# Kernel optimization log

Hardware: AMD Instinct MI355X
Metric: run time of the kernel (lower is better)

## Reference

```python
import jax, jax.numpy as jnp
import numpy as np

N = 33554432  # 2**25 activations, 128 MB fp32
K = 1024      # winners kept


def setup_inputs() -> dict:
    key = jax.random.key(0)
    inputs = jax.random.normal(key, (N,), dtype=jnp.float32)
    return {"inputs": inputs, "k": K}


def reference(inputs, k):
    # k-th largest value = threshold (original: tf.sort desc, take element k-1)
    topk_vals, _ = jax.lax.top_k(inputs, k)
    threshold = topk_vals[k - 1]
    # zero out everything strictly below the threshold
    return jnp.where(inputs < threshold, jnp.zeros_like(inputs), inputs)
```

## Files before the change

kernel.cpp:

```cpp
#include <hip/hip_runtime.h>
#include <stdint.h>


#define HIST_BINS 4096
#define CTRL_OFF  HIST_BINS
#define CAND_OFF  (HIST_BINS + 16)

typedef float f32x4 __attribute__((ext_vector_type(4)));

__device__ __forceinline__ uint32_t f2key(float x) {
  uint32_t u = __float_as_uint(x);
  return (u & 0x80000000u) ? ~u : (u | 0x80000000u);
}
__device__ __forceinline__ float key2f(uint32_t k) {
  uint32_t u = (k & 0x80000000u) ? (k & 0x7fffffffu) : ~k;
  return __uint_as_float(u);
}

__global__ void k_hist(const float4* __restrict__ in, int n4, int ntail,
                       const float* __restrict__ in_s,
                       uint32_t* __restrict__ ghist) {
  __shared__ uint32_t lh[HIST_BINS];
  for (int i = threadIdx.x; i < HIST_BINS; i += blockDim.x) lh[i] = 0;
  __syncthreads();
  int stride = gridDim.x * blockDim.x;
  for (int i = blockIdx.x * blockDim.x + threadIdx.x; i < n4; i += stride) {
    float4 v = in[i];
    atomicAdd(&lh[f2key(v.x) >> 20], 1u);
    atomicAdd(&lh[f2key(v.y) >> 20], 1u);
    atomicAdd(&lh[f2key(v.z) >> 20], 1u);
    atomicAdd(&lh[f2key(v.w) >> 20], 1u);
  }
  if (blockIdx.x == 0 && (int)threadIdx.x < ntail)
    atomicAdd(&lh[f2key(in_s[n4 * 4 + threadIdx.x]) >> 20], 1u);
  __syncthreads();
  for (int i = threadIdx.x; i < HIST_BINS; i += blockDim.x) {
    uint32_t c = lh[i];
    if (c) atomicAdd(&ghist[i], c);
  }
}

__global__ void k_select_bucket(const uint32_t* __restrict__ gh,
                                const int* __restrict__ kptr,
                                uint32_t* __restrict__ ctrl) {
  __shared__ uint32_t chunk[256];
  const int CPT = HIST_BINS / 256;
  int t = threadIdx.x;
  uint32_t s = 0;
  for (int i = 0; i < CPT; i++) s += gh[t * CPT + i];
  chunk[t] = s;
  __syncthreads();
  if (t == 0) {
    uint32_t K = (uint32_t)kptr[0];
    uint32_t above = 0;
    int sel = 0;
    for (int c = 255; c >= 0; c--) {
      if (above + chunk[c] >= K) { sel = c; break; }
      above += chunk[c];
    }
    int bsel = sel * CPT;
    for (int b = sel * CPT + CPT - 1; b >= sel * CPT; b--) {
      uint32_t c = gh[b];
      if (above + c >= K) { bsel = b; break; }
      above += c;
    }
    ctrl[1] = (uint32_t)bsel;
    ctrl[2] = K - above;
  }
}

__global__ void k_apply_gather(const float4* __restrict__ in,
                               float4* __restrict__ out, int n4, int ntail,
                               const float* __restrict__ in_s,
                               float* __restrict__ out_s,
                               uint32_t* __restrict__ ctrl,
                               uint32_t* __restrict__ keys,
                               uint32_t* __restrict__ idxs, uint32_t cap) {
  uint32_t sel = ctrl[1];
  int stride = gridDim.x * blockDim.x;
  for (int i = blockIdx.x * blockDim.x + threadIdx.x; i < n4; i += stride) {
    f32x4 vv = __builtin_nontemporal_load((const f32x4*)&in[i]);
    uint32_t k0 = f2key(vv.x), k1 = f2key(vv.y), k2 = f2key(vv.z), k3 = f2key(vv.w);
    uint32_t b0 = k0 >> 20, b1 = k1 >> 20, b2 = k2 >> 20, b3 = k3 >> 20;
    f32x4 r;
    r.x = (b0 > sel) ? vv.x : 0.0f;
    r.y = (b1 > sel) ? vv.y : 0.0f;
    r.z = (b2 > sel) ? vv.z : 0.0f;
    r.w = (b3 > sel) ? vv.w : 0.0f;
    if (b0 == sel) { uint32_t p = atomicAdd(&ctrl[0], 1u); if (p < cap) { keys[p] = k0; idxs[p] = 4u * i + 0u; } }
    if (b1 == sel) { uint32_t p = atomicAdd(&ctrl[0], 1u); if (p < cap) { keys[p] = k1; idxs[p] = 4u * i + 1u; } }
    if (b2 == sel) { uint32_t p = atomicAdd(&ctrl[0], 1u); if (p < cap) { keys[p] = k2; idxs[p] = 4u * i + 2u; } }
    if (b3 == sel) { uint32_t p = atomicAdd(&ctrl[0], 1u); if (p < cap) { keys[p] = k3; idxs[p] = 4u * i + 3u; } }
    __builtin_nontemporal_store(r, (f32x4*)&out[i]);
  }
  if (blockIdx.x == 0 && (int)threadIdx.x < ntail) {
    int j = n4 * 4 + threadIdx.x;
    float x = in_s[j];
    uint32_t kk = f2key(x);
    uint32_t bb = kk >> 20;
    out_s[j] = (bb > sel) ? x : 0.0f;
    if (bb == sel) { uint32_t p = atomicAdd(&ctrl[0], 1u); if (p < cap) { keys[p] = kk; idxs[p] = (uint32_t)j; } }
  }
}

__global__ void __launch_bounds__(1024) k_final(uint32_t* __restrict__ ctrl,
                                                const uint32_t* __restrict__ keys,
                                                const uint32_t* __restrict__ idxs,
                                                uint32_t cap,
                                                float* __restrict__ out_s) {
  __shared__ uint32_t sh[8192];
  __shared__ uint32_t cnt[16];
  __shared__ uint32_t s_p, s_want;
  int t = threadIdx.x;
  uint32_t n = ctrl[0]; if (n > cap) n = cap;
  bool useLds = (n <= 8192);
  if (useLds) for (uint32_t i = t; i < n; i += blockDim.x) sh[i] = keys[i];
  if (t == 0) { s_p = ctrl[1] << 20; s_want = ctrl[2]; }
  __syncthreads();
  uint32_t p = s_p;
  for (int d = 4; d >= 0; d--) {
    if (t < 16) cnt[t] = 0;
    __syncthreads();
    int sh_hi = 4 * d + 4;
    uint32_t pref = p >> sh_hi;
    for (uint32_t i = t; i < n; i += blockDim.x) {
      uint32_t kk = useLds ? sh[i] : keys[i];
      if ((kk >> sh_hi) == pref) atomicAdd(&cnt[(kk >> (4 * d)) & 15u], 1u);
    }
    __syncthreads();
    if (t == 0) {
      uint32_t want = s_want, acc = 0;
      uint32_t v = 0;
      for (int x = 15; x >= 0; x--) {
        if (acc + cnt[x] >= want) { v = (uint32_t)x; break; }
        acc += cnt[x];
      }
      s_p = p | (v << (4 * d));
      s_want = want - acc;
    }
    __syncthreads();
    p = s_p;
  }
  if (t == 0) ctrl[3] = __float_as_uint(key2f(p));
  for (uint32_t i = t; i < n; i += blockDim.x) {
    uint32_t kk = useLds ? sh[i] : keys[i];
    if (kk >= p) out_s[idxs[i]] = key2f(kk);
  }
}

extern "C" void kernel_launch(void* const* d_in, const int* in_sizes, int n_in,
                              void* d_out, int out_size, void* d_ws, size_t ws_size,
                              hipStream_t stream) {
  const float* in = (const float*)d_in[0];
  const int* kptr = (const int*)d_in[1];
  float* out = (float*)d_out;
  int n = in_sizes[0];
  int n4 = n >> 2;
  int ntail = n & 3;

  uint32_t* ws = (uint32_t*)d_ws;
  uint32_t* ghist = ws;
  uint32_t* ctrl = ws + CTRL_OFF;
  size_t ws_words = ws_size / 4;
  uint32_t cap = 0;
  if (ws_words > CAND_OFF + 2) cap = (uint32_t)((ws_words - CAND_OFF) / 2);
  uint32_t* keys = ws + CAND_OFF;
  uint32_t* idxs = keys + cap;

  hipMemsetAsync(d_ws, 0, CAND_OFF * sizeof(uint32_t), stream);

  k_hist<<<1024, 256, 0, stream>>>((const float4*)in, n4, ntail, in, ghist);
  k_select_bucket<<<1, 256, 0, stream>>>(ghist, kptr, ctrl);
  k_apply_gather<<<4096, 256, 0, stream>>>((const float4*)in, (float4*)out,
                                           n4, ntail, in, out, ctrl, keys, idxs, cap);
  k_final<<<1, 1024, 0, stream>>>(ctrl, keys, idxs, cap, out);
}
```

Before: 264.9 us.

## Fuse select and final kernels into preceding passes via last-block-done pattern

Merges the single-block bucket-select kernel into the histogram kernel and the single-block final refine kernel into the apply/gather kernel, using an atomic completion counter so the last finishing block does the serial work. It also rotates the global histogram flush order per block to spread atomic contention, changes the histogram launch to 512x512, and switches the apply pass input from a nontemporal load to a normal load. This removes two kernel launches and their gaps. In exchange, the final refinement now runs with 256 threads reading candidates from global memory instead of 1024 threads working from LDS.

```diff
diff --git a/kernel.cpp b/kernel.cpp
--- a/kernel.cpp
+++ b/kernel.cpp
@@ -17,10 +17,16 @@
   return __uint_as_float(u);
 }
 
-__global__ void k_hist(const float4* __restrict__ in, int n4, int ntail,
-                       const float* __restrict__ in_s,
-                       uint32_t* __restrict__ ghist) {
+__device__ __forceinline__ uint32_t agent_load(const uint32_t* p) {
+  return __hip_atomic_load(p, __ATOMIC_RELAXED, __HIP_MEMORY_SCOPE_AGENT);
+}
+
+__global__ void __launch_bounds__(512) k_hist_select(
+    const float4* __restrict__ in, int n4, int ntail,
+    const float* __restrict__ in_s, const int* __restrict__ kptr,
+    uint32_t* __restrict__ ghist, uint32_t* __restrict__ ctrl) {
   __shared__ uint32_t lh[HIST_BINS];
+  __shared__ uint32_t s_done;
   for (int i = threadIdx.x; i < HIST_BINS; i += blockDim.x) lh[i] = 0;
   __syncthreads();
   int stride = gridDim.x * blockDim.x;
@@ -35,32 +41,37 @@
     atomicAdd(&lh[f2key(in_s[n4 * 4 + threadIdx.x]) >> 20], 1u);
   __syncthreads();
   for (int i = threadIdx.x; i < HIST_BINS; i += blockDim.x) {
-    uint32_t c = lh[i];
-    if (c) atomicAdd(&ghist[i], c);
+    int j = (i + (blockIdx.x << 6)) & (HIST_BINS - 1);
+    uint32_t c = lh[j];
+    if (c) atomicAdd(&ghist[j], c);
   }
-}
+  __threadfence();
+  if (threadIdx.x == 0)
+    s_done = __hip_atomic_fetch_add(&ctrl[4], 1u, __ATOMIC_ACQ_REL,
+                                    __HIP_MEMORY_SCOPE_AGENT);
+  __syncthreads();
+  if (s_done != (uint32_t)gridDim.x - 1u) return;
+  __threadfence();
 
-__global__ void k_select_bucket(const uint32_t* __restrict__ gh,
-                                const int* __restrict__ kptr,
-                                uint32_t* __restrict__ ctrl) {
-  __shared__ uint32_t chunk[256];
+  int t = threadIdx.x;
   const int CPT = HIST_BINS / 256;
-  int t = threadIdx.x;
-  uint32_t s = 0;
-  for (int i = 0; i < CPT; i++) s += gh[t * CPT + i];
-  chunk[t] = s;
+  if (t < 256) {
+    uint32_t s = 0;
+    for (int i = 0; i < CPT; i++) s += agent_load(&ghist[t * CPT + i]);
+    lh[t] = s;
+  }
   __syncthreads();
   if (t == 0) {
     uint32_t K = (uint32_t)kptr[0];
     uint32_t above = 0;
     int sel = 0;
     for (int c = 255; c >= 0; c--) {
-      if (above + chunk[c] >= K) { sel = c; break; }
-      above += chunk[c];
+      if (above + lh[c] >= K) { sel = c; break; }
+      above += lh[c];
     }
     int bsel = sel * CPT;
     for (int b = sel * CPT + CPT - 1; b >= sel * CPT; b--) {
-      uint32_t c = gh[b];
+      uint32_t c = agent_load(&ghist[b]);
       if (above + c >= K) { bsel = b; break; }
       above += c;
     }
@@ -69,17 +80,17 @@
   }
 }
 
-__global__ void k_apply_gather(const float4* __restrict__ in,
-                               float4* __restrict__ out, int n4, int ntail,
-                               const float* __restrict__ in_s,
-                               float* __restrict__ out_s,
-                               uint32_t* __restrict__ ctrl,
-                               uint32_t* __restrict__ keys,
-                               uint32_t* __restrict__ idxs, uint32_t cap) {
+__global__ void __launch_bounds__(256) k_apply_final(
+    const float4* __restrict__ in, float4* __restrict__ out, int n4, int ntail,
+    const float* __restrict__ in_s, float* __restrict__ out_s,
+    uint32_t* __restrict__ ctrl, uint32_t* __restrict__ keys,
+    uint32_t* __restrict__ idxs, uint32_t cap) {
+  __shared__ uint32_t cnt[16];
+  __shared__ uint32_t s_done, s_p, s_want;
   uint32_t sel = ctrl[1];
   int stride = gridDim.x * blockDim.x;
   for (int i = blockIdx.x * blockDim.x + threadIdx.x; i < n4; i += stride) {
-    f32x4 vv = __builtin_nontemporal_load((const f32x4*)&in[i]);
+    f32x4 vv = *(const f32x4*)&in[i];
     uint32_t k0 = f2key(vv.x), k1 = f2key(vv.y), k2 = f2key(vv.z), k3 = f2key(vv.w);
     uint32_t b0 = k0 >> 20, b1 = k1 >> 20, b2 = k2 >> 20, b3 = k3 >> 20;
     f32x4 r;
@@ -101,36 +112,30 @@
     out_s[j] = (bb > sel) ? x : 0.0f;
     if (bb == sel) { uint32_t p = atomicAdd(&ctrl[0], 1u); if (p < cap) { keys[p] = kk; idxs[p] = (uint32_t)j; } }
   }
-}
+  __threadfence();
+  if (threadIdx.x == 0)
+    s_done = __hip_atomic_fetch_add(&ctrl[5], 1u, __ATOMIC_ACQ_REL,
+                                    __HIP_MEMORY_SCOPE_AGENT);
+  __syncthreads();
+  if (s_done != (uint32_t)gridDim.x - 1u) return;
+  __threadfence();
 
-__global__ void __launch_bounds__(1024) k_final(uint32_t* __restrict__ ctrl,
-                                                const uint32_t* __restrict__ keys,
-                                                const uint32_t* __restrict__ idxs,
-                                                uint32_t cap,
-                                                float* __restrict__ out_s) {
-  __shared__ uint32_t sh[8192];
-  __shared__ uint32_t cnt[16];
-  __shared__ uint32_t s_p, s_want;
   int t = threadIdx.x;
-  uint32_t n = ctrl[0]; if (n > cap) n = cap;
-  bool useLds = (n <= 8192);
-  if (useLds) for (uint32_t i = t; i < n; i += blockDim.x) sh[i] = keys[i];
-  if (t == 0) { s_p = ctrl[1] << 20; s_want = ctrl[2]; }
-  __syncthreads();
-  uint32_t p = s_p;
+  uint32_t n = agent_load(&ctrl[0]); if (n > cap) n = cap;
+  uint32_t p = sel << 20;
+  uint32_t want = ctrl[2];
   for (int d = 4; d >= 0; d--) {
     if (t < 16) cnt[t] = 0;
     __syncthreads();
     int sh_hi = 4 * d + 4;
     uint32_t pref = p >> sh_hi;
     for (uint32_t i = t; i < n; i += blockDim.x) {
-      uint32_t kk = useLds ? sh[i] : keys[i];
+      uint32_t kk = agent_load(&keys[i]);
       if ((kk >> sh_hi) == pref) atomicAdd(&cnt[(kk >> (4 * d)) & 15u], 1u);
     }
     __syncthreads();
     if (t == 0) {
-      uint32_t want = s_want, acc = 0;
-      uint32_t v = 0;
+      uint32_t acc = 0, v = 0;
       for (int x = 15; x >= 0; x--) {
         if (acc + cnt[x] >= want) { v = (uint32_t)x; break; }
         acc += cnt[x];
@@ -139,12 +144,12 @@
       s_want = want - acc;
     }
     __syncthreads();
-    p = s_p;
+    p = s_p; want = s_want;
   }
   if (t == 0) ctrl[3] = __float_as_uint(key2f(p));
   for (uint32_t i = t; i < n; i += blockDim.x) {
-    uint32_t kk = useLds ? sh[i] : keys[i];
-    if (kk >= p) out_s[idxs[i]] = key2f(kk);
+    uint32_t kk = agent_load(&keys[i]);
+    if (kk >= p) out_s[agent_load(&idxs[i])] = key2f(kk);
   }
 }
 
@@ -169,9 +174,8 @@
 
   hipMemsetAsync(d_ws, 0, CAND_OFF * sizeof(uint32_t), stream);
 
-  k_hist<<<1024, 256, 0, stream>>>((const float4*)in, n4, ntail, in, ghist);
-  k_select_bucket<<<1, 256, 0, stream>>>(ghist, kptr, ctrl);
-  k_apply_gather<<<4096, 256, 0, stream>>>((const float4*)in, (float4*)out,
-                                           n4, ntail, in, out, ctrl, keys, idxs, cap);
-  k_final<<<1, 1024, 0, stream>>>(ctrl, keys, idxs, cap, out);
+  k_hist_select<<<512, 512, 0, stream>>>((const float4*)in, n4, ntail, in,
+                                         kptr, ghist, ctrl);
+  k_apply_final<<<4096, 256, 0, stream>>>((const float4*)in, (float4*)out,
+                                          n4, ntail, in, out, ctrl, keys, idxs, cap);
 }
```

Result: slower. 854.3 us (+222.4%).

## Collect speculative top candidates during histogram pass; zero output via memset

Applied to the files above, without the earlier changes.

The histogram pass now also collects every element whose key is at or above a fixed cutoff (value 3.5) into the candidate list. That cutoff fits standard-normal inputs of this size, where it should keep a few thousand candidates. The full second read-and-write pass is replaced by a memset of the output plus a scatter of the survivors in the final kernel. A fallback kernel rescans the input only when the selected bucket falls below the cutoff or the candidate count overflows the buffer, so correctness is kept for other inputs at the cost of an extra pass in that case. The final kernel's shared-memory candidate buffer is doubled to hold the larger candidate set.

```diff
diff --git a/kernel.cpp b/kernel.cpp
--- a/kernel.cpp
+++ b/kernel.cpp
@@ -5,6 +5,8 @@
 #define HIST_BINS 4096
 #define CTRL_OFF  HIST_BINS
 #define CAND_OFF  (HIST_BINS + 16)
+
+#define FILTER_KEY 0xC0600000u
 
 typedef float f32x4 __attribute__((ext_vector_type(4)));
 
@@ -17,22 +19,34 @@
   return __uint_as_float(u);
 }
 
-__global__ void k_hist(const float4* __restrict__ in, int n4, int ntail,
-                       const float* __restrict__ in_s,
-                       uint32_t* __restrict__ ghist) {
+__global__ void k_hist_filter(const float4* __restrict__ in, int n4, int ntail,
+                              const float* __restrict__ in_s,
+                              uint32_t* __restrict__ ghist,
+                              uint32_t* __restrict__ ctrl,
+                              uint32_t* __restrict__ keys,
+                              uint32_t* __restrict__ idxs, uint32_t cap) {
   __shared__ uint32_t lh[HIST_BINS];
   for (int i = threadIdx.x; i < HIST_BINS; i += blockDim.x) lh[i] = 0;
   __syncthreads();
   int stride = gridDim.x * blockDim.x;
   for (int i = blockIdx.x * blockDim.x + threadIdx.x; i < n4; i += stride) {
-    float4 v = in[i];
-    atomicAdd(&lh[f2key(v.x) >> 20], 1u);
-    atomicAdd(&lh[f2key(v.y) >> 20], 1u);
-    atomicAdd(&lh[f2key(v.z) >> 20], 1u);
-    atomicAdd(&lh[f2key(v.w) >> 20], 1u);
+    f32x4 v = __builtin_nontemporal_load((const f32x4*)&in[i]);
+    uint32_t k0 = f2key(v.x), k1 = f2key(v.y), k2 = f2key(v.z), k3 = f2key(v.w);
+    atomicAdd(&lh[k0 >> 20], 1u);
+    atomicAdd(&lh[k1 >> 20], 1u);
+    atomicAdd(&lh[k2 >> 20], 1u);
+    atomicAdd(&lh[k3 >> 20], 1u);
+    if (k0 >= FILTER_KEY) { uint32_t p = atomicAdd(&ctrl[0], 1u); if (p < cap) { keys[p] = k0; idxs[p] = 4u * i + 0u; } }
+    if (k1 >= FILTER_KEY) { uint32_t p = atomicAdd(&ctrl[0], 1u); if (p < cap) { keys[p] = k1; idxs[p] = 4u * i + 1u; } }
+    if (k2 >= FILTER_KEY) { uint32_t p = atomicAdd(&ctrl[0], 1u); if (p < cap) { keys[p] = k2; idxs[p] = 4u * i + 2u; } }
+    if (k3 >= FILTER_KEY) { uint32_t p = atomicAdd(&ctrl[0], 1u); if (p < cap) { keys[p] = k3; idxs[p] = 4u * i + 3u; } }
   }
-  if (blockIdx.x == 0 && (int)threadIdx.x < ntail)
-    atomicAdd(&lh[f2key(in_s[n4 * 4 + threadIdx.x]) >> 20], 1u);
+  if (blockIdx.x == 0 && (int)threadIdx.x < ntail) {
+    int j = n4 * 4 + threadIdx.x;
+    uint32_t kk = f2key(in_s[j]);
+    atomicAdd(&lh[kk >> 20], 1u);
+    if (kk >= FILTER_KEY) { uint32_t p = atomicAdd(&ctrl[0], 1u); if (p < cap) { keys[p] = kk; idxs[p] = (uint32_t)j; } }
+  }
   __syncthreads();
   for (int i = threadIdx.x; i < HIST_BINS; i += blockDim.x) {
     uint32_t c = lh[i];
@@ -42,7 +56,7 @@
 
 __global__ void k_select_bucket(const uint32_t* __restrict__ gh,
                                 const int* __restrict__ kptr,
-                                uint32_t* __restrict__ ctrl) {
+                                uint32_t* __restrict__ ctrl, uint32_t cap) {
   __shared__ uint32_t chunk[256];
   const int CPT = HIST_BINS / 256;
   int t = threadIdx.x;
@@ -66,40 +80,32 @@
     }
     ctrl[1] = (uint32_t)bsel;
     ctrl[2] = K - above;
+    uint32_t nc = ctrl[0];
+    bool valid = ((uint32_t)bsel >= (FILTER_KEY >> 20)) && (nc <= cap);
+    if (!valid) { ctrl[0] = 0; ctrl[6] = 1; }
+    else ctrl[6] = 0;
   }
 }
 
-__global__ void k_apply_gather(const float4* __restrict__ in,
-                               float4* __restrict__ out, int n4, int ntail,
-                               const float* __restrict__ in_s,
-                               float* __restrict__ out_s,
-                               uint32_t* __restrict__ ctrl,
-                               uint32_t* __restrict__ keys,
-                               uint32_t* __restrict__ idxs, uint32_t cap) {
+__global__ void __launch_bounds__(256) k_gather_fallback(
+    const float4* __restrict__ in, int n4, int ntail,
+    const float* __restrict__ in_s, uint32_t* __restrict__ ctrl,
+    uint32_t* __restrict__ keys, uint32_t* __restrict__ idxs, uint32_t cap) {
+  if (ctrl[6] == 0) return;
   uint32_t sel = ctrl[1];
   int stride = gridDim.x * blockDim.x;
   for (int i = blockIdx.x * blockDim.x + threadIdx.x; i < n4; i += stride) {
-    f32x4 vv = __builtin_nontemporal_load((const f32x4*)&in[i]);
-    uint32_t k0 = f2key(vv.x), k1 = f2key(vv.y), k2 = f2key(vv.z), k3 = f2key(vv.w);
-    uint32_t b0 = k0 >> 20, b1 = k1 >> 20, b2 = k2 >> 20, b3 = k3 >> 20;
-    f32x4 r;
-    r.x = (b0 > sel) ? vv.x : 0.0f;
-    r.y = (b1 > sel) ? vv.y : 0.0f;
-    r.z = (b2 > sel) ? vv.z : 0.0f;
-    r.w = (b3 > sel) ? vv.w : 0.0f;
-    if (b0 == sel) { uint32_t p = atomicAdd(&ctrl[0], 1u); if (p < cap) { keys[p] = k0; idxs[p] = 4u * i + 0u; } }
-    if (b1 == sel) { uint32_t p = atomicAdd(&ctrl[0], 1u); if (p < cap) { keys[p] = k1; idxs[p] = 4u * i + 1u; } }
-    if (b2 == sel) { uint32_t p = atomicAdd(&ctrl[0], 1u); if (p < cap) { keys[p] = k2; idxs[p] = 4u * i + 2u; } }
-    if (b3 == sel) { uint32_t p = atomicAdd(&ctrl[0], 1u); if (p < cap) { keys[p] = k3; idxs[p] = 4u * i + 3u; } }
-    __builtin_nontemporal_store(r, (f32x4*)&out[i]);
+    f32x4 v = *(const f32x4*)&in[i];
+    uint32_t k0 = f2key(v.x), k1 = f2key(v.y), k2 = f2key(v.z), k3 = f2key(v.w);
+    if ((k0 >> 20) >= sel) { uint32_t p = atomicAdd(&ctrl[0], 1u); if (p < cap) { keys[p] = k0; idxs[p] = 4u * i + 0u; } }
+    if ((k1 >> 20) >= sel) { uint32_t p = atomicAdd(&ctrl[0], 1u); if (p < cap) { keys[p] = k1; idxs[p] = 4u * i + 1u; } }
+    if ((k2 >> 20) >= sel) { uint32_t p = atomicAdd(&ctrl[0], 1u); if (p < cap) { keys[p] = k2; idxs[p] = 4u * i + 2u; } }
+    if ((k3 >> 20) >= sel) { uint32_t p = atomicAdd(&ctrl[0], 1u); if (p < cap) { keys[p] = k3; idxs[p] = 4u * i + 3u; } }
   }
   if (blockIdx.x == 0 && (int)threadIdx.x < ntail) {
     int j = n4 * 4 + threadIdx.x;
-    float x = in_s[j];
-    uint32_t kk = f2key(x);
-    uint32_t bb = kk >> 20;
-    out_s[j] = (bb > sel) ? x : 0.0f;
-    if (bb == sel) { uint32_t p = atomicAdd(&ctrl[0], 1u); if (p < cap) { keys[p] = kk; idxs[p] = (uint32_t)j; } }
+    uint32_t kk = f2key(in_s[j]);
+    if ((kk >> 20) >= sel) { uint32_t p = atomicAdd(&ctrl[0], 1u); if (p < cap) { keys[p] = kk; idxs[p] = (uint32_t)j; } }
   }
 }
 
@@ -108,12 +114,12 @@
                                                 const uint32_t* __restrict__ idxs,
                                                 uint32_t cap,
                                                 float* __restrict__ out_s) {
-  __shared__ uint32_t sh[8192];
+  __shared__ uint32_t sh[16384];
   __shared__ uint32_t cnt[16];
   __shared__ uint32_t s_p, s_want;
   int t = threadIdx.x;
   uint32_t n = ctrl[0]; if (n > cap) n = cap;
-  bool useLds = (n <= 8192);
+  bool useLds = (n <= 16384);
   if (useLds) for (uint32_t i = t; i < n; i += blockDim.x) sh[i] = keys[i];
   if (t == 0) { s_p = ctrl[1] << 20; s_want = ctrl[2]; }
   __syncthreads();
@@ -168,10 +174,12 @@
   uint32_t* idxs = keys + cap;
 
   hipMemsetAsync(d_ws, 0, CAND_OFF * sizeof(uint32_t), stream);
+  hipMemsetAsync(d_out, 0, (size_t)out_size, stream);
 
-  k_hist<<<1024, 256, 0, stream>>>((const float4*)in, n4, ntail, in, ghist);
-  k_select_bucket<<<1, 256, 0, stream>>>(ghist, kptr, ctrl);
-  k_apply_gather<<<4096, 256, 0, stream>>>((const float4*)in, (float4*)out,
-                                           n4, ntail, in, out, ctrl, keys, idxs, cap);
+  k_hist_filter<<<1024, 256, 0, stream>>>((const float4*)in, n4, ntail, in,
+                                          ghist, ctrl, keys, idxs, cap);
+  k_select_bucket<<<1, 256, 0, stream>>>(ghist, kptr, ctrl, cap);
+  k_gather_fallback<<<2048, 256, 0, stream>>>((const float4*)in, n4, ntail, in,
+                                              ctrl, keys, idxs, cap);
   k_final<<<1, 1024, 0, stream>>>(ctrl, keys, idxs, cap, out);
 }
```

New measurement: 305.4 us. +15.3%, slower.
